# Kernel optimization log

Hardware: AMD Instinct MI355X
Metric: run time of the kernel (lower is better)

Reference implementation:

```python
import jax, jax.numpy as jnp
import numpy as np

BINS = 10
LOSS_WEIGHT = 1.0


def setup_inputs() -> dict:
    key = jax.random.key(0)
    k1, k2 = jax.random.split(key)
    N, C = 32768, 1024
    pred = jax.random.normal(k1, (N, C), dtype=jnp.float32)
    target = jax.random.randint(k2, (N,), 0, C, dtype=jnp.int32)
    return {"pred": pred, "target": target}


def reference(pred, target):
    N, C = pred.shape
    # one-hot target (torch scatter_ of 1 at label index)
    t = jax.nn.one_hot(target, C, dtype=pred.dtype)  # [N, C]
    # gradient norm g = |sigmoid(pred).detach() - target|, in [0, 1]
    g = jnp.abs(jax.nn.sigmoid(jax.lax.stop_gradient(pred)) - t)
    # all samples valid (label_weight=None -> ones); tot = max(sum(valid), 1)
    tot = jnp.asarray(N * C, dtype=pred.dtype)
    # edges = arange(bins+1)/bins with edges[-1] += 1e-6: bin = floor(g*bins),
    # g == 1.0 falls in last bin -> clip to bins-1
    bin_idx = jnp.clip((g * BINS).astype(jnp.int32), 0, BINS - 1)  # [N, C]
    counts = jnp.bincount(bin_idx.ravel(), length=BINS).astype(pred.dtype)  # [BINS]
    nonempty = counts > 0
    n = jnp.maximum(jnp.sum(nonempty).astype(pred.dtype), 1.0)
    # per-bin weight tot/num_in_bin for nonempty bins, then divide by n
    w_bin = jnp.where(nonempty, tot / jnp.maximum(counts, 1.0), 0.0) / n
    weights = w_bin[bin_idx]  # gather back to [N, C]
    # stable BCE-with-logits, weighted, reduction='sum'
    bce = jnp.maximum(pred, 0.0) - pred * t + jnp.log1p(jnp.exp(-jnp.abs(pred)))
    loss = jnp.sum(weights * bce) / tot
    return loss * LOSS_WEIGHT
```

## Files before the change

kernel.cpp:

```cpp
#include <hip/hip_runtime.h>
#include <math.h>


#define BLK 256
#define GRID 2048

typedef float v4f __attribute__((ext_vector_type(4)));

__device__ __constant__ float kT[9] = {
    -2.1972246f, -1.3862944f, -0.84729786f, -0.40546511f, 0.0f,
    0.40546511f, 0.84729786f, 1.3862944f, 2.1972246f};

__device__ __forceinline__ void wave_red(float& v) {
#pragma unroll
    for (int off = 32; off > 0; off >>= 1) v += __shfl_down(v, off, 64);
}
__device__ __forceinline__ void wave_red(int& v) {
#pragma unroll
    for (int off = 32; off > 0; off >>= 1) v += __shfl_down(v, off, 64);
}

__device__ __forceinline__ void upd(float x, float (&S)[10], int (&cnt)[9]) {
    float en = __expf(-fabsf(x));
    float bce = fmaxf(x, 0.0f) + __logf(1.0f + en);
    S[0] += bce;
#pragma unroll
    for (int q = 0; q < 9; ++q) {
        bool b = (x >= kT[q]);
        S[q + 1] += b ? bce : 0.0f;
        cnt[q] += b ? 1 : 0;
    }
}

__device__ __forceinline__ void upd_corr(float p, float (&S)[10], int (&cnt)[9]) {
    float en = __expf(-fabsf(p));
    float l1p = __logf(1.0f + en);
    float bf = fmaxf(p, 0.0f) + l1p;
    float bt = fmaxf(-p, 0.0f) + l1p;
    S[0] += bt - bf;
#pragma unroll
    for (int q = 0; q < 9; ++q) {
        bool btq = (-p >= kT[q]);
        bool bfq = (p >= kT[q]);
        S[q + 1] += (btq ? bt : 0.0f) - (bfq ? bf : 0.0f);
        cnt[q] += (btq ? 1 : 0) - (bfq ? 1 : 0);
    }
}

__global__ __launch_bounds__(BLK, 8) void ghmc_pass1(
    const float* __restrict__ pred, const int* __restrict__ target,
    float* __restrict__ blk, unsigned total4, unsigned totalNC, int N, int C) {
    float S[10];
    int cnt[9];
#pragma unroll
    for (int i = 0; i < 10; ++i) S[i] = 0.0f;
#pragma unroll
    for (int i = 0; i < 9; ++i) cnt[i] = 0;

    unsigned tid = blockIdx.x * blockDim.x + threadIdx.x;
    unsigned stride = gridDim.x * blockDim.x;
    const v4f* p4 = (const v4f*)pred;

    unsigned v = tid;
    for (; v + stride < total4; v += 2u * stride) {
        v4f a = p4[v];
        v4f b = p4[v + stride];
        upd(a[0], S, cnt);
        upd(a[1], S, cnt);
        upd(a[2], S, cnt);
        upd(a[3], S, cnt);
        upd(b[0], S, cnt);
        upd(b[1], S, cnt);
        upd(b[2], S, cnt);
        upd(b[3], S, cnt);
    }
    for (; v < total4; v += stride) {
        v4f a = p4[v];
        upd(a[0], S, cnt);
        upd(a[1], S, cnt);
        upd(a[2], S, cnt);
        upd(a[3], S, cnt);
    }

    if (tid == 0) {
        for (unsigned e = total4 << 2; e < totalNC; ++e) upd(pred[e], S, cnt);
    }

    int row = (int)tid;
    if (row < N) {
        int t = target[row];
        float p = pred[(unsigned)row * (unsigned)C + (unsigned)t];
        upd_corr(p, S, cnt);
    }

#pragma unroll
    for (int i = 0; i < 10; ++i) wave_red(S[i]);
#pragma unroll
    for (int i = 0; i < 9; ++i) wave_red(cnt[i]);

    __shared__ float sS[BLK / 64][10];
    __shared__ int sC[BLK / 64][9];
    int wid = threadIdx.x >> 6;
    int lane = threadIdx.x & 63;
    if (lane == 0) {
#pragma unroll
        for (int i = 0; i < 10; ++i) sS[wid][i] = S[i];
#pragma unroll
        for (int i = 0; i < 9; ++i) sC[wid][i] = cnt[i];
    }
    __syncthreads();
    if (threadIdx.x == 0) {
        const int nw = BLK / 64;
        float o[19];
#pragma unroll
        for (int i = 0; i < 10; ++i) {
            float a = 0.0f;
            for (int w = 0; w < nw; ++w) a += sS[w][i];
            o[i] = a;
        }
#pragma unroll
        for (int i = 0; i < 9; ++i) {
            int a = 0;
            for (int w = 0; w < nw; ++w) a += sC[w][i];
            o[10 + i] = (float)a;
        }
        float* dst = blk + (unsigned)blockIdx.x * 20u;
#pragma unroll
        for (int i = 0; i < 19; ++i) dst[i] = o[i];
    }
}

__global__ __launch_bounds__(256) void ghmc_pass2(
    const float* __restrict__ blk, float* __restrict__ out, int nblocks,
    float totalNC) {
    float P[19];
#pragma unroll
    for (int i = 0; i < 19; ++i) P[i] = 0.0f;

    for (int b = threadIdx.x; b < nblocks; b += 256) {
        const float* src = blk + (unsigned)b * 20u;
#pragma unroll
        for (int i = 0; i < 19; ++i) P[i] += src[i];
    }
#pragma unroll
    for (int i = 0; i < 19; ++i) wave_red(P[i]);

    __shared__ float sP[4][19];
    int wid = threadIdx.x >> 6;
    int lane = threadIdx.x & 63;
    if (lane == 0) {
#pragma unroll
        for (int i = 0; i < 19; ++i) sP[wid][i] = P[i];
    }
    __syncthreads();
    if (threadIdx.x == 0) {
        float Sv[11], Cv[11];
        for (int i = 0; i < 19; ++i) {
            float a = 0.0f;
            for (int w = 0; w < 4; ++w) a += sP[w][i];
            P[i] = a;
        }
        for (int i = 0; i < 10; ++i) Sv[i] = P[i];
        Sv[10] = 0.0f;
        Cv[0] = totalNC;
        for (int i = 1; i < 10; ++i) Cv[i] = P[9 + i];
        Cv[10] = 0.0f;

        int nonempty = 0;
        for (int b = 0; b < 10; ++b)
            if (Cv[b] - Cv[b + 1] > 0.5f) nonempty++;
        float n = fmaxf((float)nonempty, 1.0f);

        float loss = 0.0f;
        for (int b = 0; b < 10; ++b) {
            float c = Cv[b] - Cv[b + 1];
            if (c > 0.5f) loss += (Sv[b] - Sv[b + 1]) / (c * n);
        }
        out[0] = loss;
    }
}

extern "C" void kernel_launch(void* const* d_in, const int* in_sizes, int n_in,
                              void* d_out, int out_size, void* d_ws, size_t ws_size,
                              hipStream_t stream) {
    const float* pred = (const float*)d_in[0];
    const int* target = (const int*)d_in[1];
    int NC = in_sizes[0];
    int N = in_sizes[1];
    int C = NC / N;
    unsigned total4 = (unsigned)(NC / 4);

    int blocks = GRID;
    size_t per_block = 20 * sizeof(float);
    if (ws_size < (size_t)blocks * per_block) {
        size_t maxb = ws_size / per_block;
        blocks = (int)(maxb > 0 ? maxb : 1);
    }

    float* blkbuf = (float*)d_ws;

    ghmc_pass1<<<blocks, BLK, 0, stream>>>(pred, target, blkbuf, total4,
                                           (unsigned)NC, N, C);
    ghmc_pass2<<<1, 256, 0, stream>>>(blkbuf, (float*)d_out, blocks, (float)NC);
}
```

Measured before the change: 201.0 us.

## Replace log with polynomial, inline thresholds, software-pipeline loads, vectorize pass2

Replaces __logf(1+e) with a degree-5 polynomial approximation of log1p on [0,1] and moves the threshold constants from constant memory into compile-time immediates. The main streaming loop is software-pipelined so the next pair of v4f loads is issued before the current pair is processed. Pass2 now reads the padded 20-float per-block records as v4f vectors. The aim is to cut the per-element transcendental cost and hide memory latency, at the price of a small approximation error in the BCE term and higher register pressure.

```diff
diff --git a/kernel.cpp b/kernel.cpp
--- a/kernel.cpp
+++ b/kernel.cpp
@@ -7,10 +7,6 @@
 
 typedef float v4f __attribute__((ext_vector_type(4)));
 
-__device__ __constant__ float kT[9] = {
-    -2.1972246f, -1.3862944f, -0.84729786f, -0.40546511f, 0.0f,
-    0.40546511f, 0.84729786f, 1.3862944f, 2.1972246f};
-
 __device__ __forceinline__ void wave_red(float& v) {
 #pragma unroll
     for (int off = 32; off > 0; off >>= 1) v += __shfl_down(v, off, 64);
@@ -20,31 +16,53 @@
     for (int off = 32; off > 0; off >>= 1) v += __shfl_down(v, off, 64);
 }
 
+__device__ __forceinline__ float log1p_poly(float t) {
+    float r = 0.03215845f;
+    r = fmaf(r, t, -0.13606275f);
+    r = fmaf(r, t, 0.28947478f);
+    r = fmaf(r, t, -0.49190896f);
+    r = fmaf(r, t, 0.99949556f);
+    return r * t;
+}
+
 __device__ __forceinline__ void upd(float x, float (&S)[10], int (&cnt)[9]) {
+    const float T0 = -2.1972246f, T1 = -1.3862944f, T2 = -0.84729786f,
+                T3 = -0.40546511f, T4 = 0.0f, T5 = 0.40546511f,
+                T6 = 0.84729786f, T7 = 1.3862944f, T8 = 2.1972246f;
     float en = __expf(-fabsf(x));
-    float bce = fmaxf(x, 0.0f) + __logf(1.0f + en);
+    float bce = fmaxf(x, 0.0f) + log1p_poly(en);
     S[0] += bce;
+    const float Tk[9] = {T0, T1, T2, T3, T4, T5, T6, T7, T8};
 #pragma unroll
     for (int q = 0; q < 9; ++q) {
-        bool b = (x >= kT[q]);
+        bool b = (x >= Tk[q]);
         S[q + 1] += b ? bce : 0.0f;
         cnt[q] += b ? 1 : 0;
     }
 }
 
 __device__ __forceinline__ void upd_corr(float p, float (&S)[10], int (&cnt)[9]) {
+    const float Tk[9] = {-2.1972246f, -1.3862944f, -0.84729786f, -0.40546511f,
+                         0.0f, 0.40546511f, 0.84729786f, 1.3862944f, 2.1972246f};
     float en = __expf(-fabsf(p));
-    float l1p = __logf(1.0f + en);
+    float l1p = log1p_poly(en);
     float bf = fmaxf(p, 0.0f) + l1p;
     float bt = fmaxf(-p, 0.0f) + l1p;
     S[0] += bt - bf;
 #pragma unroll
     for (int q = 0; q < 9; ++q) {
-        bool btq = (-p >= kT[q]);
-        bool bfq = (p >= kT[q]);
+        bool btq = (-p >= Tk[q]);
+        bool bfq = (p >= Tk[q]);
         S[q + 1] += (btq ? bt : 0.0f) - (bfq ? bf : 0.0f);
         cnt[q] += (btq ? 1 : 0) - (bfq ? 1 : 0);
     }
+}
+
+__device__ __forceinline__ void upd4(const v4f& a, float (&S)[10], int (&cnt)[9]) {
+    upd(a[0], S, cnt);
+    upd(a[1], S, cnt);
+    upd(a[2], S, cnt);
+    upd(a[3], S, cnt);
 }
 
 __global__ __launch_bounds__(BLK, 8) void ghmc_pass1(
@@ -57,39 +75,40 @@
 #pragma unroll
     for (int i = 0; i < 9; ++i) cnt[i] = 0;
 
-    unsigned tid = blockIdx.x * blockDim.x + threadIdx.x;
-    unsigned stride = gridDim.x * blockDim.x;
+    unsigned gtid = blockIdx.x * BLK + threadIdx.x;
+    unsigned stride = gridDim.x * BLK;
     const v4f* p4 = (const v4f*)pred;
 
-    unsigned v = tid;
-    for (; v + stride < total4; v += 2u * stride) {
+    unsigned v = gtid;
+    if (v + stride < total4) {
         v4f a = p4[v];
         v4f b = p4[v + stride];
-        upd(a[0], S, cnt);
-        upd(a[1], S, cnt);
-        upd(a[2], S, cnt);
-        upd(a[3], S, cnt);
-        upd(b[0], S, cnt);
-        upd(b[1], S, cnt);
-        upd(b[2], S, cnt);
-        upd(b[3], S, cnt);
+        unsigned nv = v + 2u * stride;
+        while (nv + stride < total4) {
+            v4f a2 = p4[nv];
+            v4f b2 = p4[nv + stride];
+            upd4(a, S, cnt);
+            upd4(b, S, cnt);
+            a = a2;
+            b = b2;
+            nv += 2u * stride;
+        }
+        upd4(a, S, cnt);
+        upd4(b, S, cnt);
+        v = nv;
     }
     for (; v < total4; v += stride) {
         v4f a = p4[v];
-        upd(a[0], S, cnt);
-        upd(a[1], S, cnt);
-        upd(a[2], S, cnt);
-        upd(a[3], S, cnt);
-    }
-
-    if (tid == 0) {
+        upd4(a, S, cnt);
+    }
+
+    if (gtid == 0) {
         for (unsigned e = total4 << 2; e < totalNC; ++e) upd(pred[e], S, cnt);
     }
 
-    int row = (int)tid;
-    if (row < N) {
-        int t = target[row];
-        float p = pred[(unsigned)row * (unsigned)C + (unsigned)t];
+    if ((int)gtid < N) {
+        int t = target[gtid];
+        float p = pred[gtid * (unsigned)C + (unsigned)t];
         upd_corr(p, S, cnt);
     }
 
@@ -111,7 +130,7 @@
     __syncthreads();
     if (threadIdx.x == 0) {
         const int nw = BLK / 64;
-        float o[19];
+        float o[20];
 #pragma unroll
         for (int i = 0; i < 10; ++i) {
             float a = 0.0f;
@@ -124,38 +143,45 @@
             for (int w = 0; w < nw; ++w) a += sC[w][i];
             o[10 + i] = (float)a;
         }
+        o[19] = 0.0f;
         float* dst = blk + (unsigned)blockIdx.x * 20u;
 #pragma unroll
-        for (int i = 0; i < 19; ++i) dst[i] = o[i];
+        for (int i = 0; i < 20; ++i) dst[i] = o[i];
     }
 }
 
 __global__ __launch_bounds__(256) void ghmc_pass2(
     const float* __restrict__ blk, float* __restrict__ out, int nblocks,
     float totalNC) {
-    float P[19];
-#pragma unroll
-    for (int i = 0; i < 19; ++i) P[i] = 0.0f;
-
+    float P[20];
+#pragma unroll
+    for (int i = 0; i < 20; ++i) P[i] = 0.0f;
+
+    const v4f* b4 = (const v4f*)blk;
     for (int b = threadIdx.x; b < nblocks; b += 256) {
-        const float* src = blk + (unsigned)b * 20u;
-#pragma unroll
-        for (int i = 0; i < 19; ++i) P[i] += src[i];
-    }
-#pragma unroll
-    for (int i = 0; i < 19; ++i) wave_red(P[i]);
-
-    __shared__ float sP[4][19];
+#pragma unroll
+        for (int j = 0; j < 5; ++j) {
+            v4f c = b4[b * 5 + j];
+            P[4 * j + 0] += c[0];
+            P[4 * j + 1] += c[1];
+            P[4 * j + 2] += c[2];
+            P[4 * j + 3] += c[3];
+        }
+    }
+#pragma unroll
+    for (int i = 0; i < 20; ++i) wave_red(P[i]);
+
+    __shared__ float sP[4][20];
     int wid = threadIdx.x >> 6;
     int lane = threadIdx.x & 63;
     if (lane == 0) {
 #pragma unroll
-        for (int i = 0; i < 19; ++i) sP[wid][i] = P[i];
+        for (int i = 0; i < 20; ++i) sP[wid][i] = P[i];
     }
     __syncthreads();
     if (threadIdx.x == 0) {
         float Sv[11], Cv[11];
-        for (int i = 0; i < 19; ++i) {
+        for (int i = 0; i < 20; ++i) {
             float a = 0.0f;
             for (int w = 0; w < 4; ++w) a += sP[w][i];
             P[i] = a;
```

After: 216.2 us. +7.6%, slower.
